# Kernel optimization log

Measured on AMD Instinct MI355X. Metric: run time of the kernel, lower is better.

## Reference

```python
import jax, jax.numpy as jnp
import numpy as np

EPS = 1e-5

def setup_inputs() -> dict:
    key = jax.random.key(0)
    ks = jax.random.split(key, 12)
    B = 4096
    x = jax.random.normal(ks[0], (B, 28, 28, 1), dtype=jnp.float32)
    # BatchNorm1d(1) affine params (applied per-channel over active sites)
    bn_gamma = jnp.ones((1,), jnp.float32)
    bn_beta = jnp.zeros((1,), jnp.float32)
    # SubMConv2d weights, HWIO layout
    w1 = jax.random.normal(ks[1], (3, 3, 1, 32), jnp.float32) * 0.1
    b1 = jax.random.normal(ks[2], (32,), jnp.float32) * 0.01
    w2 = jax.random.normal(ks[3], (3, 3, 32, 64), jnp.float32) * 0.05
    b2 = jax.random.normal(ks[4], (64,), jnp.float32) * 0.01
    # FC layers (torch Linear: y = x @ W.T + b)
    fcw1 = jax.random.normal(ks[5], (128, 14 * 14 * 64), jnp.float32) * 0.01
    fcb1 = jnp.zeros((128,), jnp.float32)
    fcw2 = jax.random.normal(ks[6], (10, 128), jnp.float32) * 0.05
    fcb2 = jnp.zeros((10,), jnp.float32)
    return {"x": x, "bn_gamma": bn_gamma, "bn_beta": bn_beta,
            "w1": w1, "b1": b1, "w2": w2, "b2": b2,
            "fcw1": fcw1, "fcb1": fcb1, "fcw2": fcw2, "fcb2": fcb2}

def _subm_conv(feat, mask, w, b):
    # Submanifold conv: inactive inputs are zero (already masked), and the
    # output coordinate set equals the input active set -> mask the output.
    y = jax.lax.conv_general_dilated(
        feat, w, window_strides=(1, 1), padding='SAME',
        dimension_numbers=('NHWC', 'HWIO', 'NHWC'))
    return jnp.where(mask, y + b, 0.0)

def reference(x, bn_gamma, bn_beta, w1, b1, w2, b2, fcw1, fcb1, fcw2, fcb2):
    # from_dense: active sites are locations with nonzero feature. [B,28,28,1]
    mask = (x != 0)  # single channel -> site mask [B,28,28,1]
    maskf = mask.astype(x.dtype)
    # BatchNorm1d(1) on the [N_active, 1] sparse feature tensor (batch stats)
    n = jnp.maximum(maskf.sum(), 1.0)
    mean = (x * maskf).sum() / n
    var = (jnp.square(x - mean) * maskf).sum() / n
    feat = maskf * (bn_gamma * (x - mean) * jax.lax.rsqrt(var + EPS) + bn_beta)
    # SubMConv2d(1,32,3,1) + ReLU
    h = jax.nn.relu(_subm_conv(feat, mask, w1, b1))  # [B,28,28,32]
    # SubMConv2d(32,64,3,1) + ReLU
    h = jax.nn.relu(_subm_conv(h, mask, w2, b2))     # [B,28,28,64]
    # SparseMaxPool2d(2,2): max over active sites per window; since values are
    # post-ReLU (>=0) and inactive sites hold 0, dense maxpool is exact, and
    # fully-inactive windows correctly yield 0 after ToDense.
    h = jax.lax.reduce_window(h, -jnp.inf, jax.lax.max,
                              (1, 2, 2, 1), (1, 2, 2, 1), 'VALID')  # [B,14,14,64]
    # ToDense gives NCHW [B,64,14,14]; torch.flatten uses C-major order
    h = jnp.transpose(h, (0, 3, 1, 2)).reshape(h.shape[0], -1)  # [B,12544]
    # dropout1/dropout2 are identity in eval mode
    h = jax.nn.relu(h @ fcw1.T + fcb1)
    logits = h @ fcw2.T + fcb2
    return jax.nn.log_softmax(logits, axis=1)
```

## Files before the change

### kernel.cpp

```cpp
#include <hip/hip_runtime.h>
#include <stdint.h>

typedef unsigned short u16;
typedef unsigned int u32;
typedef __attribute__((ext_vector_type(8))) short bf16x8;
typedef __attribute__((ext_vector_type(4))) float f32x4;

__device__ __forceinline__ u16 f2bf(float f) {
    u32 u = __float_as_uint(f);
    u32 r = (u + 0x7fffu + ((u >> 16) & 1u)) >> 16;
    return (u16)r;
}

__device__ __forceinline__ void gload16(const u16* src, u16* dst) {
    __builtin_amdgcn_global_load_lds(
        (const __attribute__((address_space(1))) u32*)src,
        (__attribute__((address_space(3))) u32*)dst, 16, 0, 0);
}

__global__ __launch_bounds__(256) void k_stats(const float* __restrict__ x, int n,
                                               float* __restrict__ stats) {
    int t = blockIdx.x * 256 + threadIdx.x;
    int stride = gridDim.x * 256;
    float c = 0.f, s = 0.f, ss = 0.f;
    for (int i = t; i < n; i += stride) {
        float v = x[i];
        if (v != 0.f) { c += 1.f; s += v; ss = fmaf(v, v, ss); }
    }
    for (int off = 32; off > 0; off >>= 1) {
        c  += __shfl_down(c, off);
        s  += __shfl_down(s, off);
        ss += __shfl_down(ss, off);
    }
    __shared__ float red[3][4];
    int lane = threadIdx.x & 63, wv = threadIdx.x >> 6;
    if (lane == 0) { red[0][wv] = c; red[1][wv] = s; red[2][wv] = ss; }
    __syncthreads();
    if (threadIdx.x == 0) {
        atomicAdd(&stats[0], red[0][0] + red[0][1] + red[0][2] + red[0][3]);
        atomicAdd(&stats[1], red[1][0] + red[1][1] + red[1][2] + red[1][3]);
        atomicAdd(&stats[2], red[2][0] + red[2][1] + red[2][2] + red[2][3]);
    }
}

__global__ void k_finalize(const float* __restrict__ g, const float* __restrict__ b,
                           float* __restrict__ stats) {
    float n = stats[0]; if (n < 1.f) n = 1.f;
    float mean = stats[1] / n;
    float var = stats[2] / n - mean * mean;
    if (var < 0.f) var = 0.f;
    float scale = g[0] * rsqrtf(var + 1e-5f);
    stats[4] = scale;
    stats[5] = b[0] - mean * scale;
}

__global__ __launch_bounds__(256) void k_prepall(const float* __restrict__ w2,
    const float* __restrict__ fcw1, u16* __restrict__ w2b, u16* __restrict__ fcw1b, int n)
{
    int i = blockIdx.x * 256 + threadIdx.x;
    if (i < 9 * 64 * 32) {
        int tap = i >> 11, rem = i & 2047, co = rem >> 5, ci = rem & 31;
        w2b[i] = f2bf(w2[tap * 2048 + ci * 64 + co]);
    }
    if (i < n) fcw1b[i] = f2bf(fcw1[i]);
}

__global__ __launch_bounds__(256, 2) void k_conv(const float* __restrict__ x,
    const float* __restrict__ w1, const float* __restrict__ b1,
    const u16* __restrict__ w2b, const float* __restrict__ b2,
    const float* __restrict__ stats, u16* __restrict__ pooled)
{
    __shared__ u16 h1[28928];
    __shared__ float feat[30][30];
    __shared__ unsigned char mk[784];
    __shared__ unsigned char pm[200];
    const int t = threadIdx.x;
    const int b = blockIdx.x;
    const int lane = t & 63;
    const int wv = t >> 6;
    const int lg = lane >> 4;
    const int lr = lane & 15;

    const float scale = stats[4], shift = stats[5];

    for (int i = t; i < 14464; i += 256) ((u32*)h1)[i] = 0u;
    for (int i = t; i < 900; i += 256) (&feat[0][0])[i] = 0.f;
    __syncthreads();

    const float* xb = x + (size_t)b * 784;
    for (int i = t; i < 784; i += 256) {
        float v = xb[i];
        bool m = (v != 0.f);
        mk[i] = m ? 1 : 0;
        int h = i / 28, w = i - h * 28;
        feat[h + 1][w + 1] = m ? fmaf(v, scale, shift) : 0.f;
    }
    __syncthreads();

    if (t < 196) {
        int rr = t / 14, cc = t - rr * 14;
        int base = rr * 56 + cc * 2;
        pm[t] = (unsigned char)(mk[base] | (mk[base + 1] << 1)
              | (mk[base + 28] << 2) | (mk[base + 29] << 3));
    }

    {
        const int cp = (t >> 4) & 3;
        const int pxg = (t & 15) | ((t >> 6) << 4);
        float wk[9][8], bs[8];
        {
            float4 b0 = *(const float4*)(b1 + cp * 8);
            float4 b4 = *(const float4*)(b1 + cp * 8 + 4);
            bs[0]=b0.x; bs[1]=b0.y; bs[2]=b0.z; bs[3]=b0.w;
            bs[4]=b4.x; bs[5]=b4.y; bs[6]=b4.z; bs[7]=b4.w;
        }
        #pragma unroll
        for (int j = 0; j < 9; ++j) {
            float4 w0 = *(const float4*)(w1 + j * 32 + cp * 8);
            float4 w4 = *(const float4*)(w1 + j * 32 + cp * 8 + 4);
            wk[j][0]=w0.x; wk[j][1]=w0.y; wk[j][2]=w0.z; wk[j][3]=w0.w;
            wk[j][4]=w4.x; wk[j][5]=w4.y; wk[j][6]=w4.z; wk[j][7]=w4.w;
        }
        char* hb = (char*)h1 + cp * 14464;
        for (int px = pxg; px < 784; px += 64) {
            if (!mk[px]) continue;
            int h = px / 28, w = px - h * 28;
            float a[8];
            #pragma unroll
            for (int c = 0; c < 8; ++c) a[c] = bs[c];
            #pragma unroll
            for (int kh = 0; kh < 3; ++kh)
                #pragma unroll
                for (int kw = 0; kw < 3; ++kw) {
                    float f = feat[h + kh][w + kw];
                    #pragma unroll
                    for (int c = 0; c < 8; ++c) a[c] = fmaf(f, wk[kh * 3 + kw][c], a[c]);
                }
            u32 q0 = (u32)f2bf(fmaxf(a[0], 0.f)) | ((u32)f2bf(fmaxf(a[1], 0.f)) << 16);
            u32 q1 = (u32)f2bf(fmaxf(a[2], 0.f)) | ((u32)f2bf(fmaxf(a[3], 0.f)) << 16);
            u32 q2 = (u32)f2bf(fmaxf(a[4], 0.f)) | ((u32)f2bf(fmaxf(a[5], 0.f)) << 16);
            u32 q3 = (u32)f2bf(fmaxf(a[6], 0.f)) | ((u32)f2bf(fmaxf(a[7], 0.f)) << 16);
            *(uint4*)(hb + ((h + 1) * 30 + (w + 1)) * 16) = make_uint4(q0, q1, q2, q3);
        }
    }
    __syncthreads();

    bf16x8 wf[9][4];
    #pragma unroll
    for (int tap = 0; tap < 9; ++tap)
        #pragma unroll
        for (int nt = 0; nt < 4; ++nt)
            wf[tap][nt] = *(const bf16x8*)(w2b + tap * 2048 + (nt * 16 + lr) * 32 + lg * 8);
    float bias2[4];
    #pragma unroll
    for (int nt = 0; nt < 4; ++nt) bias2[nt] = b2[nt * 16 + lr];

    const int cb = wv & 1;
    const int r0 = wv >> 1;
    const char* gb = (const char*)h1 + lg * 14464 + (cb * 16 + lr) * 16;
    const bool store_ok = !(cb == 1 && lg == 3);
    const int pc0 = cb * 8 + lg * 2;
    u16* poolb = pooled + (size_t)b * 12544;

    #pragma unroll 1
    for (int i = 0; i < 7; ++i) {
        const int r = r0 + 2 * i;
        const char* ab = gb + 960 * r;
        bf16x8 a0[3], a1[3], a2[3], a3[3];
        #pragma unroll
        for (int kw = 0; kw < 3; ++kw) {
            a0[kw] = *(const bf16x8*)(ab + kw * 16);
            a1[kw] = *(const bf16x8*)(ab + 480 + kw * 16);
            a2[kw] = *(const bf16x8*)(ab + 960 + kw * 16);
        }
        f32x4 acc0[4], acc1[4];
        #pragma unroll
        for (int nt = 0; nt < 4; ++nt) {
            acc0[nt] = (f32x4){bias2[nt], bias2[nt], bias2[nt], bias2[nt]};
            acc1[nt] = acc0[nt];
        }
        #pragma unroll
        for (int nt = 0; nt < 4; ++nt)
            #pragma unroll
            for (int kw = 0; kw < 3; ++kw) {
                acc0[nt] = __builtin_amdgcn_mfma_f32_16x16x32_bf16(a0[kw], wf[kw][nt], acc0[nt], 0, 0, 0);
                acc0[nt] = __builtin_amdgcn_mfma_f32_16x16x32_bf16(a1[kw], wf[3 + kw][nt], acc0[nt], 0, 0, 0);
                acc0[nt] = __builtin_amdgcn_mfma_f32_16x16x32_bf16(a2[kw], wf[6 + kw][nt], acc0[nt], 0, 0, 0);
            }
        #pragma unroll
        for (int kw = 0; kw < 3; ++kw)
            a3[kw] = *(const bf16x8*)(ab + 1440 + kw * 16);
        #pragma unroll
        for (int nt = 0; nt < 4; ++nt)
            #pragma unroll
            for (int kw = 0; kw < 3; ++kw) {
                acc1[nt] = __builtin_amdgcn_mfma_f32_16x16x32_bf16(a1[kw], wf[kw][nt], acc1[nt], 0, 0, 0);
                acc1[nt] = __builtin_amdgcn_mfma_f32_16x16x32_bf16(a2[kw], wf[3 + kw][nt], acc1[nt], 0, 0, 0);
                acc1[nt] = __builtin_amdgcn_mfma_f32_16x16x32_bf16(a3[kw], wf[6 + kw][nt], acc1[nt], 0, 0, 0);
            }

        if (store_ok) {
            u32 pmw = *(const u16*)&pm[r * 14 + pc0];
            float m00 = (pmw & 1u)    ? 1.f : 0.f, m01 = (pmw & 2u)    ? 1.f : 0.f;
            float m10 = (pmw & 4u)    ? 1.f : 0.f, m11 = (pmw & 8u)    ? 1.f : 0.f;
            float n00 = (pmw & 256u)  ? 1.f : 0.f, n01 = (pmw & 512u)  ? 1.f : 0.f;
            float n10 = (pmw & 1024u) ? 1.f : 0.f, n11 = (pmw & 2048u) ? 1.f : 0.f;
            #pragma unroll
            for (int nt = 0; nt < 4; ++nt) {
                float p0 = fmaxf(fmaxf(fmaxf(acc0[nt][0], 0.f) * m00, fmaxf(acc0[nt][1], 0.f) * m01),
                                 fmaxf(fmaxf(acc1[nt][0], 0.f) * m10, fmaxf(acc1[nt][1], 0.f) * m11));
                float p1 = fmaxf(fmaxf(fmaxf(acc0[nt][2], 0.f) * n00, fmaxf(acc0[nt][3], 0.f) * n01),
                                 fmaxf(fmaxf(acc1[nt][2], 0.f) * n10, fmaxf(acc1[nt][3], 0.f) * n11));
                *(u32*)&poolb[(nt * 16 + lr) * 196 + r * 14 + pc0] =
                    (u32)f2bf(p0) | ((u32)f2bf(p1) << 16);
            }
        }
    }
}

__global__ __launch_bounds__(256, 4) void k_fc1(const u16* __restrict__ pooled,
    const u16* __restrict__ fcw1b, float* __restrict__ fc1, int M)
{
    __shared__ u16 Asm[8 * 64 * 8];
    __shared__ u16 Bsm[8 * 128 * 8];
    const int t = threadIdx.x;
    const int m0 = blockIdx.x * 64;
    const int kbase = blockIdx.y * 1792;
    const int lane = t & 63;
    const int wv = t >> 6;
    const int lg = lane >> 4, lr = lane & 15;
    const int wm = wv & 1, wn = wv >> 1;

    const int ia0 = t, ia1 = t + 256;
    const u16* as0 = pooled + (size_t)(m0 + (ia0 & 63)) * 12544 + (ia0 >> 6) * 8 + kbase;
    const u16* as1 = pooled + (size_t)(m0 + (ia1 & 63)) * 12544 + (ia1 >> 6) * 8 + kbase;
    const u16* bs0 = fcw1b + (size_t)(t & 127) * 12544 + ((t >> 7) + 0) * 8 + kbase;
    const u16* bs1 = fcw1b + (size_t)(t & 127) * 12544 + ((t >> 7) + 2) * 8 + kbase;
    const u16* bs2 = fcw1b + (size_t)(t & 127) * 12544 + ((t >> 7) + 4) * 8 + kbase;
    const u16* bs3 = fcw1b + (size_t)(t & 127) * 12544 + ((t >> 7) + 6) * 8 + kbase;
    u16* ad0 = &Asm[(size_t)ia0 * 8];
    u16* ad1 = &Asm[(size_t)ia1 * 8];
    u16* bd0 = &Bsm[(size_t)(t + 0) * 8];
    u16* bd1 = &Bsm[(size_t)(t + 256) * 8];
    u16* bd2 = &Bsm[(size_t)(t + 512) * 8];
    u16* bd3 = &Bsm[(size_t)(t + 768) * 8];

    f32x4 acc[2][4];
    #pragma unroll
    for (int mi = 0; mi < 2; ++mi)
        #pragma unroll
        for (int ni = 0; ni < 4; ++ni) acc[mi][ni] = (f32x4){0.f, 0.f, 0.f, 0.f};

    for (int s = 0; s < 28; ++s) {
        const int kk = s * 64;
        __syncthreads();
        gload16(as0 + kk, ad0);
        gload16(as1 + kk, ad1);
        gload16(bs0 + kk, bd0);
        gload16(bs1 + kk, bd1);
        gload16(bs2 + kk, bd2);
        gload16(bs3 + kk, bd3);
        asm volatile("s_waitcnt vmcnt(0)" ::: "memory");
        __syncthreads();
        #pragma unroll
        for (int ks = 0; ks < 2; ++ks) {
            bf16x8 a[2], bfr[4];
            #pragma unroll
            for (int mi = 0; mi < 2; ++mi)
                a[mi] = *(const bf16x8*)&Asm[(((ks * 4 + lg) * 64) + wm * 32 + mi * 16 + lr) * 8];
            #pragma unroll
            for (int ni = 0; ni < 4; ++ni)
                bfr[ni] = *(const bf16x8*)&Bsm[(((ks * 4 + lg) * 128) + wn * 64 + ni * 16 + lr) * 8];
            #pragma unroll
            for (int mi = 0; mi < 2; ++mi)
                #pragma unroll
                for (int ni = 0; ni < 4; ++ni)
                    acc[mi][ni] = __builtin_amdgcn_mfma_f32_16x16x32_bf16(a[mi], bfr[ni], acc[mi][ni], 0, 0, 0);
        }
    }

    #pragma unroll
    for (int mi = 0; mi < 2; ++mi)
        #pragma unroll
        for (int ni = 0; ni < 4; ++ni)
            #pragma unroll
            for (int q = 0; q < 4; ++q) {
                int m = m0 + wm * 32 + mi * 16 + lg * 4 + q;
                int n = wn * 64 + ni * 16 + lr;
                atomicAdd(&fc1[(size_t)m * 128 + n], acc[mi][ni][q]);
            }
}

__global__ __launch_bounds__(256) void k_fc2(const float* __restrict__ fc1,
    const float* __restrict__ fcb1, const float* __restrict__ fcw2,
    const float* __restrict__ fcb2, float* __restrict__ out, int M)
{
    __shared__ float red[8][32][10];
    const int t = threadIdx.x;
    const int ml = t & 31, kq = t >> 5;
    const int m = blockIdx.x * 32 + ml;
    float acc[10];
    #pragma unroll
    for (int c = 0; c < 10; ++c) acc[c] = 0.f;
    const float* fp = fc1 + (size_t)m * 128 + kq * 16;
    #pragma unroll
    for (int j = 0; j < 16; j += 4) {
        float4 v4 = *(const float4*)(fp + j);
        float vv[4] = {v4.x, v4.y, v4.z, v4.w};
        #pragma unroll
        for (int u = 0; u < 4; ++u) {
            int k = kq * 16 + j + u;
            float v = fmaxf(vv[u] + fcb1[k], 0.f);
            #pragma unroll
            for (int c = 0; c < 10; ++c) acc[c] = fmaf(v, fcw2[c * 128 + k], acc[c]);
        }
    }
    #pragma unroll
    for (int c = 0; c < 10; ++c) red[kq][ml][c] = acc[c];
    __syncthreads();
    if (kq == 0) {
        float lgt[10];
        #pragma unroll
        for (int c = 0; c < 10; ++c) {
            float sv = 0.f;
            #pragma unroll
            for (int s = 0; s < 8; ++s) sv += red[s][ml][c];
            lgt[c] = sv + fcb2[c];
        }
        float mx = lgt[0];
        #pragma unroll
        for (int c = 1; c < 10; ++c) mx = fmaxf(mx, lgt[c]);
        float se = 0.f;
        #pragma unroll
        for (int c = 0; c < 10; ++c) se += expf(lgt[c] - mx);
        float lse = mx + logf(se);
        #pragma unroll
        for (int c = 0; c < 10; ++c) out[(size_t)m * 10 + c] = lgt[c] - lse;
    }
}

extern "C" void kernel_launch(void* const* d_in, const int* in_sizes, int n_in,
                              void* d_out, int out_size, void* d_ws, size_t ws_size,
                              hipStream_t stream) {
    const float* x     = (const float*)d_in[0];
    const float* gamma = (const float*)d_in[1];
    const float* beta  = (const float*)d_in[2];
    const float* w1    = (const float*)d_in[3];
    const float* b1    = (const float*)d_in[4];
    const float* w2    = (const float*)d_in[5];
    const float* b2    = (const float*)d_in[6];
    const float* fcw1  = (const float*)d_in[7];
    const float* fcb1  = (const float*)d_in[8];
    const float* fcw2  = (const float*)d_in[9];
    const float* fcb2  = (const float*)d_in[10];
    float* out = (float*)d_out;

    const int B = in_sizes[0] / 784;

    float* stats  = (float*)d_ws;
    u16*   w2b    = (u16*)((char*)d_ws + 256);
    float* fc1    = (float*)((char*)d_ws + 256);
    u16*   pooled = (u16*)((char*)d_ws + 256 + (size_t)B * 128 * 4);
    u16*   fcw1b  = (u16*)((char*)d_ws + 256 + (size_t)B * 128 * 4 + (size_t)B * 12544 * 2);

    hipMemsetAsync(stats, 0, 32, stream);
    k_stats<<<1024, 256, 0, stream>>>(x, B * 784, stats);
    k_finalize<<<1, 1, 0, stream>>>(gamma, beta, stats);
    k_prepall<<<(128 * 12544 + 255) / 256, 256, 0, stream>>>(w2, fcw1, w2b, fcw1b, 128 * 12544);
    k_conv<<<B, 256, 0, stream>>>(x, w1, b1, w2b, b2, stats, pooled);
    hipMemsetAsync(fc1, 0, (size_t)B * 128 * 4, stream);
    k_fc1<<<dim3(B / 64, 7), 256, 0, stream>>>(pooled, fcw1b, fc1, B);
    k_fc2<<<B / 32, 256, 0, stream>>>(fc1, fcb1, fcw2, fcb2, out, B);
}
```

Measured before the change: 350.0 us.

## Replace fc1 atomics with split-K partial slabs, restructure conv1, use packed bf16 converts

fc1 split-K blocks now each write their partial sums to a separate slab, and fc2 adds the seven slabs together. This removes the atomicAdds and the memset of fc1, at the cost of more workspace and extra reads in fc2. conv1 is restructured so each thread walks a half row with a sliding 3x3 window in registers and multiplies by the mask instead of branching. Only the halo of the h1 buffer is zeroed now, fcw1 is converted with float4 loads, and scalar bf16 rounding is replaced by the hardware packed convert instruction.

```diff
diff --git a/kernel.cpp b/kernel.cpp
--- a/kernel.cpp
+++ b/kernel.cpp
@@ -10,6 +10,12 @@
     u32 u = __float_as_uint(f);
     u32 r = (u + 0x7fffu + ((u >> 16) & 1u)) >> 16;
     return (u16)r;
+}
+
+__device__ __forceinline__ u32 cvtpk(float lo, float hi) {
+    u32 r;
+    asm("v_cvt_pk_bf16_f32 %0, %1, %2" : "=v"(r) : "v"(lo), "v"(hi));
+    return r;
 }
 
 __device__ __forceinline__ void gload16(const u16* src, u16* dst) {
@@ -55,14 +61,17 @@
 }
 
 __global__ __launch_bounds__(256) void k_prepall(const float* __restrict__ w2,
-    const float* __restrict__ fcw1, u16* __restrict__ w2b, u16* __restrict__ fcw1b, int n)
+    const float* __restrict__ fcw1, u16* __restrict__ w2b, u16* __restrict__ fcw1b, int n4)
 {
     int i = blockIdx.x * 256 + threadIdx.x;
     if (i < 9 * 64 * 32) {
         int tap = i >> 11, rem = i & 2047, co = rem >> 5, ci = rem & 31;
         w2b[i] = f2bf(w2[tap * 2048 + ci * 64 + co]);
     }
-    if (i < n) fcw1b[i] = f2bf(fcw1[i]);
+    if (i < n4) {
+        float4 v = *(const float4*)(fcw1 + (size_t)i * 4);
+        *(uint2*)(fcw1b + (size_t)i * 4) = make_uint2(cvtpk(v.x, v.y), cvtpk(v.z, v.w));
+    }
 }
 
 __global__ __launch_bounds__(256, 2) void k_conv(const float* __restrict__ x,
@@ -83,8 +92,19 @@
 
     const float scale = stats[4], shift = stats[5];
 
-    for (int i = t; i < 14464; i += 256) ((u32*)h1)[i] = 0u;
     for (int i = t; i < 900; i += 256) (&feat[0][0])[i] = 0.f;
+    if (t < 120) {
+        int slot;
+        if (t < 30)       slot = t;
+        else if (t < 60)  slot = 840 + t;
+        else if (t < 88)  slot = (t - 59) * 30;
+        else if (t < 116) slot = (t - 87) * 30 + 29;
+        else              slot = 784 + t;
+        const uint4 z = make_uint4(0u, 0u, 0u, 0u);
+        #pragma unroll
+        for (int g = 0; g < 4; ++g)
+            *(uint4*)&h1[g * 7232 + slot * 8] = z;
+    }
     __syncthreads();
 
     const float* xb = x + (size_t)b * 784;
@@ -107,40 +127,56 @@
     {
         const int cp = (t >> 4) & 3;
         const int pxg = (t & 15) | ((t >> 6) << 4);
-        float wk[9][8], bs[8];
-        {
-            float4 b0 = *(const float4*)(b1 + cp * 8);
-            float4 b4 = *(const float4*)(b1 + cp * 8 + 4);
-            bs[0]=b0.x; bs[1]=b0.y; bs[2]=b0.z; bs[3]=b0.w;
-            bs[4]=b4.x; bs[5]=b4.y; bs[6]=b4.z; bs[7]=b4.w;
-        }
-        #pragma unroll
-        for (int j = 0; j < 9; ++j) {
-            float4 w0 = *(const float4*)(w1 + j * 32 + cp * 8);
-            float4 w4 = *(const float4*)(w1 + j * 32 + cp * 8 + 4);
-            wk[j][0]=w0.x; wk[j][1]=w0.y; wk[j][2]=w0.z; wk[j][3]=w0.w;
-            wk[j][4]=w4.x; wk[j][5]=w4.y; wk[j][6]=w4.z; wk[j][7]=w4.w;
-        }
-        char* hb = (char*)h1 + cp * 14464;
-        for (int px = pxg; px < 784; px += 64) {
-            if (!mk[px]) continue;
-            int h = px / 28, w = px - h * 28;
-            float a[8];
-            #pragma unroll
-            for (int c = 0; c < 8; ++c) a[c] = bs[c];
-            #pragma unroll
-            for (int kh = 0; kh < 3; ++kh)
+        if (pxg < 56) {
+            const int hh = 1 + (pxg >> 1);
+            const int wb = (pxg & 1) * 14;
+            float wk[9][8], bs[8];
+            {
+                float4 b0 = *(const float4*)(b1 + cp * 8);
+                float4 b4 = *(const float4*)(b1 + cp * 8 + 4);
+                bs[0]=b0.x; bs[1]=b0.y; bs[2]=b0.z; bs[3]=b0.w;
+                bs[4]=b4.x; bs[5]=b4.y; bs[6]=b4.z; bs[7]=b4.w;
+            }
+            #pragma unroll
+            for (int j = 0; j < 9; ++j) {
+                float4 w0 = *(const float4*)(w1 + j * 32 + cp * 8);
+                float4 w4 = *(const float4*)(w1 + j * 32 + cp * 8 + 4);
+                wk[j][0]=w0.x; wk[j][1]=w0.y; wk[j][2]=w0.z; wk[j][3]=w0.w;
+                wk[j][4]=w4.x; wk[j][5]=w4.y; wk[j][6]=w4.z; wk[j][7]=w4.w;
+            }
+            char* hb = (char*)h1 + cp * 14464 + (hh * 30 + wb + 1) * 16;
+            const int pxbase = (hh - 1) * 28 + wb;
+            float c0[3], c1[3], c2[3];
+            #pragma unroll
+            for (int r = 0; r < 3; ++r) {
+                c0[r] = feat[hh - 1 + r][wb + 0];
+                c1[r] = feat[hh - 1 + r][wb + 1];
+            }
+            #pragma unroll 2
+            for (int j = 0; j < 14; ++j) {
                 #pragma unroll
-                for (int kw = 0; kw < 3; ++kw) {
-                    float f = feat[h + kh][w + kw];
+                for (int r = 0; r < 3; ++r) c2[r] = feat[hh - 1 + r][wb + j + 2];
+                float a[8];
+                #pragma unroll
+                for (int c = 0; c < 8; ++c) a[c] = bs[c];
+                #pragma unroll
+                for (int r = 0; r < 3; ++r) {
                     #pragma unroll
-                    for (int c = 0; c < 8; ++c) a[c] = fmaf(f, wk[kh * 3 + kw][c], a[c]);
+                    for (int c = 0; c < 8; ++c) {
+                        a[c] = fmaf(c0[r], wk[r * 3 + 0][c], a[c]);
+                        a[c] = fmaf(c1[r], wk[r * 3 + 1][c], a[c]);
+                        a[c] = fmaf(c2[r], wk[r * 3 + 2][c], a[c]);
+                    }
                 }
-            u32 q0 = (u32)f2bf(fmaxf(a[0], 0.f)) | ((u32)f2bf(fmaxf(a[1], 0.f)) << 16);
-            u32 q1 = (u32)f2bf(fmaxf(a[2], 0.f)) | ((u32)f2bf(fmaxf(a[3], 0.f)) << 16);
-            u32 q2 = (u32)f2bf(fmaxf(a[4], 0.f)) | ((u32)f2bf(fmaxf(a[5], 0.f)) << 16);
-            u32 q3 = (u32)f2bf(fmaxf(a[6], 0.f)) | ((u32)f2bf(fmaxf(a[7], 0.f)) << 16);
-            *(uint4*)(hb + ((h + 1) * 30 + (w + 1)) * 16) = make_uint4(q0, q1, q2, q3);
+                float mf = mk[pxbase + j] ? 1.f : 0.f;
+                u32 q0 = cvtpk(fmaxf(a[0], 0.f) * mf, fmaxf(a[1], 0.f) * mf);
+                u32 q1 = cvtpk(fmaxf(a[2], 0.f) * mf, fmaxf(a[3], 0.f) * mf);
+                u32 q2 = cvtpk(fmaxf(a[4], 0.f) * mf, fmaxf(a[5], 0.f) * mf);
+                u32 q3 = cvtpk(fmaxf(a[6], 0.f) * mf, fmaxf(a[7], 0.f) * mf);
+                *(uint4*)(hb + j * 16) = make_uint4(q0, q1, q2, q3);
+                #pragma unroll
+                for (int r = 0; r < 3; ++r) { c0[r] = c1[r]; c1[r] = c2[r]; }
+            }
         }
     }
     __syncthreads();
@@ -211,15 +247,14 @@
                                  fmaxf(fmaxf(acc1[nt][0], 0.f) * m10, fmaxf(acc1[nt][1], 0.f) * m11));
                 float p1 = fmaxf(fmaxf(fmaxf(acc0[nt][2], 0.f) * n00, fmaxf(acc0[nt][3], 0.f) * n01),
                                  fmaxf(fmaxf(acc1[nt][2], 0.f) * n10, fmaxf(acc1[nt][3], 0.f) * n11));
-                *(u32*)&poolb[(nt * 16 + lr) * 196 + r * 14 + pc0] =
-                    (u32)f2bf(p0) | ((u32)f2bf(p1) << 16);
+                *(u32*)&poolb[(nt * 16 + lr) * 196 + r * 14 + pc0] = cvtpk(p0, p1);
             }
         }
     }
 }
 
 __global__ __launch_bounds__(256, 4) void k_fc1(const u16* __restrict__ pooled,
-    const u16* __restrict__ fcw1b, float* __restrict__ fc1, int M)
+    const u16* __restrict__ fcw1b, float* __restrict__ fc1p, int M)
 {
     __shared__ u16 Asm[8 * 64 * 8];
     __shared__ u16 Bsm[8 * 128 * 8];
@@ -279,6 +314,7 @@
         }
     }
 
+    float* outp = fc1p + (size_t)blockIdx.y * M * 128;
     #pragma unroll
     for (int mi = 0; mi < 2; ++mi)
         #pragma unroll
@@ -287,11 +323,11 @@
             for (int q = 0; q < 4; ++q) {
                 int m = m0 + wm * 32 + mi * 16 + lg * 4 + q;
                 int n = wn * 64 + ni * 16 + lr;
-                atomicAdd(&fc1[(size_t)m * 128 + n], acc[mi][ni][q]);
-            }
-}
-
-__global__ __launch_bounds__(256) void k_fc2(const float* __restrict__ fc1,
+                outp[(size_t)m * 128 + n] = acc[mi][ni][q];
+            }
+}
+
+__global__ __launch_bounds__(256) void k_fc2(const float* __restrict__ fc1p,
     const float* __restrict__ fcb1, const float* __restrict__ fcw2,
     const float* __restrict__ fcb2, float* __restrict__ out, int M)
 {
@@ -299,13 +335,19 @@
     const int t = threadIdx.x;
     const int ml = t & 31, kq = t >> 5;
     const int m = blockIdx.x * 32 + ml;
+    const size_t slab = (size_t)M * 128;
     float acc[10];
     #pragma unroll
     for (int c = 0; c < 10; ++c) acc[c] = 0.f;
-    const float* fp = fc1 + (size_t)m * 128 + kq * 16;
+    const float* fp = fc1p + (size_t)m * 128 + kq * 16;
     #pragma unroll
     for (int j = 0; j < 16; j += 4) {
         float4 v4 = *(const float4*)(fp + j);
+        #pragma unroll
+        for (int s = 1; s < 7; ++s) {
+            float4 u4 = *(const float4*)(fp + s * slab + j);
+            v4.x += u4.x; v4.y += u4.y; v4.z += u4.z; v4.w += u4.w;
+        }
         float vv[4] = {v4.x, v4.y, v4.z, v4.w};
         #pragma unroll
         for (int u = 0; u < 4; ++u) {
@@ -356,19 +398,19 @@
     float* out = (float*)d_out;
 
     const int B = in_sizes[0] / 784;
-
-    float* stats  = (float*)d_ws;
-    u16*   w2b    = (u16*)((char*)d_ws + 256);
-    float* fc1    = (float*)((char*)d_ws + 256);
-    u16*   pooled = (u16*)((char*)d_ws + 256 + (size_t)B * 128 * 4);
-    u16*   fcw1b  = (u16*)((char*)d_ws + 256 + (size_t)B * 128 * 4 + (size_t)B * 12544 * 2);
+    char* base = (char*)d_ws;
+
+    float* stats  = (float*)base;
+    u16*   w2b    = (u16*)(base + 256);
+    float* fc1p   = (float*)(base + 37376);
+    u16*   pooled = (u16*)(base + 37376 + (size_t)7 * B * 128 * 4);
+    u16*   fcw1b  = (u16*)(base + 37376 + (size_t)7 * B * 128 * 4 + (size_t)B * 12544 * 2);
 
     hipMemsetAsync(stats, 0, 32, stream);
     k_stats<<<1024, 256, 0, stream>>>(x, B * 784, stats);
     k_finalize<<<1, 1, 0, stream>>>(gamma, beta, stats);
-    k_prepall<<<(128 * 12544 + 255) / 256, 256, 0, stream>>>(w2, fcw1, w2b, fcw1b, 128 * 12544);
+    k_prepall<<<1568, 256, 0, stream>>>(w2, fcw1, w2b, fcw1b, 128 * 12544 / 4);
     k_conv<<<B, 256, 0, stream>>>(x, w1, b1, w2b, b2, stats, pooled);
-    hipMemsetAsync(fc1, 0, (size_t)B * 128 * 4, stream);
-    k_fc1<<<dim3(B / 64, 7), 256, 0, stream>>>(pooled, fcw1b, fc1, B);
-    k_fc2<<<B / 32, 256, 0, stream>>>(fc1, fcb1, fcw2, fcb2, out, B);
-}
+    k_fc1<<<dim3(B / 64, 7), 256, 0, stream>>>(pooled, fcw1b, fc1p, B);
+    k_fc2<<<B / 32, 256, 0, stream>>>(fc1p, fcb1, fcw2, fcb2, out, B);
+}
```

Measured after the change: 323.0 us. 7.7% less time.
